# Kernel tuning notes

Measured on AMD Instinct MI355X. Metric: run time of the kernel, lower is better.

The kernel has to match this reference:

```python
import jax, jax.numpy as jnp
import numpy as np

N = 100000
NEG_SLOPE = 0.2
EPS = 1e-16


def gat_conv(x, edge_index, W, att_src, att_dst, bias, concat):
    # x: [N, Fin]; W: [Fin, H*C]; att_*: [H, C]; edge_index: [2, E] (with self loops)
    H, C = att_src.shape
    src, dst = edge_index[0], edge_index[1]
    h = (x @ W).reshape(-1, H, C)                       # [N, H, C]
    a_src = (h * att_src).sum(-1)                       # [N, H]
    a_dst = (h * att_dst).sum(-1)                       # [N, H]
    e = a_src[src] + a_dst[dst]                         # [E, H]
    e = jnp.where(e >= 0, e, NEG_SLOPE * e)             # LeakyReLU(0.2)
    # segment softmax over destination-node neighborhoods
    m = jax.ops.segment_max(e, dst, num_segments=N)     # [N, H]
    ex = jnp.exp(e - m[dst])
    denom = jax.ops.segment_sum(ex, dst, num_segments=N)
    alpha = ex / (denom[dst] + EPS)                     # [E, H]
    msg = h[src] * alpha[:, :, None]                    # [E, H, C]
    out = jax.ops.segment_sum(msg, dst, num_segments=N)  # [N, H, C]
    out = out.reshape(N, H * C) if concat else out.mean(axis=1)
    return out + bias


def setup_inputs() -> dict:
    key = jax.random.key(0)
    ks = jax.random.split(key, 10)
    Fin, Ch, Co, Hh = 256, 32, 64, 4
    E = 1600000
    x = jax.random.normal(ks[0], (N, Fin), dtype=jnp.float32)
    edge_index = jax.random.randint(ks[1], (2, E), 0, N, dtype=jnp.int64)
    s1 = 1.0 / np.sqrt(Fin)
    s2 = 1.0 / np.sqrt(Hh * Ch)
    W1 = jax.random.normal(ks[2], (Fin, Hh * Ch), dtype=jnp.float32) * s1
    att_src1 = jax.random.normal(ks[3], (Hh, Ch), dtype=jnp.float32) * (1.0 / np.sqrt(Ch))
    att_dst1 = jax.random.normal(ks[4], (Hh, Ch), dtype=jnp.float32) * (1.0 / np.sqrt(Ch))
    b1 = jnp.zeros((Hh * Ch,), dtype=jnp.float32)
    W2 = jax.random.normal(ks[5], (Hh * Ch, Co), dtype=jnp.float32) * s2
    att_src2 = jax.random.normal(ks[6], (1, Co), dtype=jnp.float32) * (1.0 / np.sqrt(Co))
    att_dst2 = jax.random.normal(ks[7], (1, Co), dtype=jnp.float32) * (1.0 / np.sqrt(Co))
    b2 = jnp.zeros((Co,), dtype=jnp.float32)
    return {"x": x, "edge_index": edge_index,
            "W1": W1, "att_src1": att_src1, "att_dst1": att_dst1, "b1": b1,
            "W2": W2, "att_src2": att_src2, "att_dst2": att_dst2, "b2": b2}


def reference(x, edge_index, W1, att_src1, att_dst1, b1, W2, att_src2, att_dst2, b2):
    # add self-loops (PyG GATConv default add_self_loops=True)
    loops = jnp.arange(N, dtype=edge_index.dtype)
    ei = jnp.concatenate([edge_index, jnp.stack([loops, loops])], axis=1)
    h = gat_conv(x, ei, W1, att_src1, att_dst1, b1, concat=True)
    h = jax.nn.elu(h)
    out = gat_conv(h, ei, W2, att_src2, att_dst2, b2, concat=False)
    return out
```

## Files before the change

kernel.cpp:

```cpp
#include <hip/hip_runtime.h>
#include <math.h>

typedef unsigned short ushort_t;
typedef unsigned int uint_t;
typedef __attribute__((ext_vector_type(8))) short short8;
typedef __attribute__((ext_vector_type(4))) float fx4;
typedef __attribute__((ext_vector_type(4))) uint_t uintx4;
typedef __attribute__((ext_vector_type(2))) uint_t uintx2;

__device__ __forceinline__ float bf16_to_f32(ushort_t u) {
    union { uint_t i; float f; } c;
    c.i = ((uint_t)u) << 16;
    return c.f;
}
__device__ __forceinline__ ushort_t f32_to_bf16(float f) {
    union { float f; uint_t i; } c;
    c.f = f;
    const uint_t x = c.i;
    return (ushort_t)((x + 0x7fffu + ((x >> 16) & 1u)) >> 16);
}
__device__ __forceinline__ void unpack_fma(uint_t w, float p, float& a0,
                                           float& a1) {
    union { uint_t i; float f; } lo, hi;
    lo.i = w << 16;
    hi.i = w & 0xffff0000u;
    a0 += p * lo.f;
    a1 += p * hi.f;
}

__global__ void convT_kernel(const float* __restrict__ W,
                             ushort_t* __restrict__ WT, int k, int m) {
    const int idx = blockIdx.x * 256 + threadIdx.x;
    if (idx >= k * m) return;
    const int mm = idx / k;
    const int kk = idx % k;
    WT[idx] = f32_to_bf16(W[(size_t)kk * m + mm]);
}

template <int TILES, bool A_F32, int K>
__global__ __launch_bounds__(256) void gemm_lds_kernel(
    const void* __restrict__ Avoid, const ushort_t* __restrict__ BT,
    ushort_t* __restrict__ C, int n) {
    constexpr int M = TILES * 16;
    constexpr int CH = K / 8;
    constexpr int NC = K / 32;
    __shared__ ushort_t lds[M * K];
    const int tid = threadIdx.x;

#pragma unroll
    for (int i = 0; i < (M * CH + 255) / 256; ++i) {
        const int idx = tid + i * 256;
        if (idx < M * CH) {
            const int row = idx / CH;
            const int c = idx - row * CH;
            *(short8*)&lds[(size_t)(row * CH + (c ^ (row & 7))) * 8] =
                *(const short8*)(BT + (size_t)row * K + c * 8);
        }
    }
    __syncthreads();

    const int wave = tid >> 6;
    const int lane = tid & 63;
    const int l15 = lane & 15;
    const int quad = lane >> 4;
    const int rowbase = blockIdx.x * 128 + wave * 32;
    const int r0 = min(rowbase + l15, n - 1);
    const int r1 = min(rowbase + 16 + l15, n - 1);
    const size_t off0 = (size_t)r0 * K + quad * 8;
    const size_t off1 = (size_t)r1 * K + quad * 8;

    fx4 acc[2][TILES];
#pragma unroll
    for (int rp = 0; rp < 2; ++rp)
#pragma unroll
        for (int t = 0; t < TILES; ++t) acc[rp][t] = (fx4){0.f, 0.f, 0.f, 0.f};

    fx4 c0a, c0b, c1a, c1b, n0a, n0b, n1a, n1b;
    short8 cb0, cb1, nb0, nb1;

    if constexpr (A_F32) {
        const float* A = (const float*)Avoid;
        c0a = *(const fx4*)(A + off0);
        c0b = *(const fx4*)(A + off0 + 4);
        c1a = *(const fx4*)(A + off1);
        c1b = *(const fx4*)(A + off1 + 4);
    } else {
        const ushort_t* A = (const ushort_t*)Avoid;
        cb0 = *(const short8*)(A + off0);
        cb1 = *(const short8*)(A + off1);
    }

#pragma unroll
    for (int kc = 0; kc < NC; ++kc) {
        if (kc + 1 < NC) {
            const int kd = (kc + 1) * 32;
            if constexpr (A_F32) {
                const float* A = (const float*)Avoid;
                n0a = *(const fx4*)(A + off0 + kd);
                n0b = *(const fx4*)(A + off0 + kd + 4);
                n1a = *(const fx4*)(A + off1 + kd);
                n1b = *(const fx4*)(A + off1 + kd + 4);
            } else {
                const ushort_t* A = (const ushort_t*)Avoid;
                nb0 = *(const short8*)(A + off0 + kd);
                nb1 = *(const short8*)(A + off1 + kd);
            }
        }
        short8 bf[TILES];
#pragma unroll
        for (int t = 0; t < TILES; ++t) {
            const int brow = t * 16 + l15;
            const int c = kc * 4 + quad;
            bf[t] = *(const short8*)&lds[(size_t)(brow * CH +
                                                  (c ^ (brow & 7))) * 8];
        }
        short8 af0, af1;
        if constexpr (A_F32) {
            union { short8 v; ushort_t u[8]; } u0, u1;
#pragma unroll
            for (int j = 0; j < 4; ++j) {
                u0.u[j] = f32_to_bf16(c0a[j]);
                u0.u[4 + j] = f32_to_bf16(c0b[j]);
                u1.u[j] = f32_to_bf16(c1a[j]);
                u1.u[4 + j] = f32_to_bf16(c1b[j]);
            }
            af0 = u0.v;
            af1 = u1.v;
        } else {
            af0 = cb0;
            af1 = cb1;
        }
#pragma unroll
        for (int t = 0; t < TILES; ++t) {
            acc[0][t] = __builtin_amdgcn_mfma_f32_16x16x32_bf16(af0, bf[t],
                                                                acc[0][t],
                                                                0, 0, 0);
            acc[1][t] = __builtin_amdgcn_mfma_f32_16x16x32_bf16(af1, bf[t],
                                                                acc[1][t],
                                                                0, 0, 0);
        }
        if (kc + 1 < NC) {
            if constexpr (A_F32) {
                c0a = n0a; c0b = n0b; c1a = n1a; c1b = n1b;
            } else {
                cb0 = nb0; cb1 = nb1;
            }
        }
    }

#pragma unroll
    for (int rp = 0; rp < 2; ++rp) {
        const int crow0 = rowbase + rp * 16 + quad * 4;
#pragma unroll
        for (int t = 0; t < TILES; ++t) {
#pragma unroll
            for (int r = 0; r < 4; ++r) {
                const int rr = crow0 + r;
                if (rr < n)
                    C[(size_t)rr * M + t * 16 + l15] =
                        f32_to_bf16(acc[rp][t][r]);
            }
        }
    }
}

template <int H, int C>
__global__ void att_kernel(const ushort_t* __restrict__ h,
                           const float* __restrict__ att_s,
                           const float* __restrict__ att_d,
                           float* __restrict__ as_, float* __restrict__ ad_,
                           int n) {
    const int idx = blockIdx.x * blockDim.x + threadIdx.x;
    if (idx >= n * H) return;
    const int node = idx / H;
    const int hh = idx % H;
    const ushort_t* hp = h + (size_t)node * H * C + hh * C;
    float s0 = 0.f, s1 = 0.f;
#pragma unroll
    for (int c = 0; c < C; ++c) {
        const float v = bf16_to_f32(hp[c]);
        s0 += v * att_s[hh * C + c];
        s1 += v * att_d[hh * C + c];
    }
    as_[idx] = s0;
    ad_[idx] = s1;
}

__global__ __launch_bounds__(1024) void hist_kernel(const int* __restrict__ dst,
                                                    int* __restrict__ histG,
                                                    int e, int chunk, int NB,
                                                    int G) {
    __shared__ int hl[512];
    for (int b = threadIdx.x; b < NB; b += 1024) hl[b] = 0;
    __syncthreads();
    const int g = blockIdx.x;
    const int lo = g * chunk;
    const int hi = min(lo + chunk, e);
    for (int i = lo + threadIdx.x; i < hi; i += 1024)
        atomicAdd(&hl[dst[i] >> 8], 1);
    __syncthreads();
    for (int b = threadIdx.x; b < NB; b += 1024) histG[b * G + g] = hl[b];
}

__global__ __launch_bounds__(1024) void scan1_kernel(const int* __restrict__ in,
                                                     int* __restrict__ out,
                                                     int* __restrict__ sums,
                                                     int n) {
    __shared__ int s[1024];
    const int t = threadIdx.x;
    const int i = blockIdx.x * 1024 + t;
    const int v = (i < n) ? in[i] : 0;
    s[t] = v;
    __syncthreads();
    for (int d = 1; d < 1024; d <<= 1) {
        const int x = (t >= d) ? s[t - d] : 0;
        __syncthreads();
        s[t] += x;
        __syncthreads();
    }
    if (i < n) out[i] = s[t] - v;
    if (t == 1023) sums[blockIdx.x] = s[1023];
}

__global__ __launch_bounds__(128) void scan2_kernel(int* sums, int nb) {
    __shared__ int s[128];
    const int t = threadIdx.x;
    const int v = (t < nb) ? sums[t] : 0;
    s[t] = v;
    __syncthreads();
    for (int d = 1; d < 128; d <<= 1) {
        const int x = (t >= d) ? s[t - d] : 0;
        __syncthreads();
        s[t] += x;
        __syncthreads();
    }
    if (t < nb) sums[t] = s[t] - v;
}

__global__ __launch_bounds__(1024) void scan3_kernel(int* __restrict__ out,
                                                     const int* __restrict__ sums,
                                                     int n) {
    const int i = blockIdx.x * 1024 + threadIdx.x;
    if (i < n) out[i] += sums[blockIdx.x];
}

__global__ __launch_bounds__(1024) void bin_kernel(const int* __restrict__ src,
                                                   const int* __restrict__ dst,
                                                   const int* __restrict__ base,
                                                   int2* __restrict__ binned,
                                                   int e, int chunk, int NB,
                                                   int G) {
    __shared__ int cur[512];
    const int g = blockIdx.x;
    for (int b = threadIdx.x; b < NB; b += 1024) cur[b] = base[b * G + g];
    __syncthreads();
    const int lo = g * chunk;
    const int hi = min(lo + chunk, e);
    for (int i = lo + threadIdx.x; i < hi; i += 1024) {
        const int d = dst[i];
        const int p = atomicAdd(&cur[d >> 8], 1);
        binned[p] = make_int2(src[i], d);
    }
}

#define BUILD_CAP 6144
__global__ __launch_bounds__(256) void build_kernel(
    const int2* __restrict__ binned, const int* __restrict__ base,
    int* __restrict__ csr, int* __restrict__ deg, int* __restrict__ offs,
    int e, int n, int NB, int G) {
    __shared__ int2 ep[BUILD_CAP];
    __shared__ int degL[256];
    __shared__ int offL[256];
    __shared__ int curL[256];
    const int b = blockIdx.x;
    const int tid = threadIdx.x;
    const int start = base[b * G];
    const int end = (b == NB - 1) ? e : base[(b + 1) * G];
    const int cnt = end - start;
    const bool stage = (cnt <= BUILD_CAP);
    degL[tid] = 0;
    if (stage)
        for (int i = tid; i < cnt; i += 256) ep[i] = binned[start + i];
    __syncthreads();
    if (stage) {
        for (int i = tid; i < cnt; i += 256) atomicAdd(&degL[ep[i].y & 255], 1);
    } else {
        for (int i = tid; i < cnt; i += 256)
            atomicAdd(&degL[binned[start + i].y & 255], 1);
    }
    __syncthreads();
    const int v = degL[tid];
    offL[tid] = v;
    __syncthreads();
    for (int d = 1; d < 256; d <<= 1) {
        const int x = (tid >= d) ? offL[tid - d] : 0;
        __syncthreads();
        offL[tid] += x;
        __syncthreads();
    }
    const int excl = offL[tid] - v;
    curL[tid] = excl;
    const int node = (b << 8) + tid;
    if (node < n) {
        deg[node] = v;
        offs[node] = start + excl;
    }
    __syncthreads();
    if (stage) {
        for (int i = tid; i < cnt; i += 256) {
            const int p = atomicAdd(&curL[ep[i].y & 255], 1);
            csr[start + p] = ep[i].x;
        }
    } else {
        for (int i = tid; i < cnt; i += 256) {
            const int2 pr = binned[start + i];
            const int p = atomicAdd(&curL[pr.y & 255], 1);
            csr[start + p] = pr.x;
        }
    }
}

template <int H, int C, bool DO_ELU, bool OUT_BF16>
__global__ __launch_bounds__(64) void agg_kernel(
    const ushort_t* __restrict__ h, const float* __restrict__ a_src,
    const float* __restrict__ a_dst, const int* __restrict__ csr,
    const int* __restrict__ offs, const int* __restrict__ deg,
    const float* __restrict__ bias, void* __restrict__ outv, int n) {
    constexpr int HC = H * C;
    constexpr int R = HC / 16;
    constexpr int RW = R / 2;
    constexpr int U = 4;
    const int lane = threadIdx.x;
    const int s = lane & 15;
    const int g = lane >> 4;
    const int dst = blockIdx.x * 4 + g;
    const int dstc = min(dst, n - 1);
    const int start = offs[dstc];
    const int dg = deg[dstc];
    const int ch0 = s * R;
    const int myh = (H > 1) ? (ch0 / C) : 0;
    const float advm = a_dst[dstc * H + myh];

    int dmax = dg;
    dmax = max(dmax, __shfl_xor(dmax, 16));
    dmax = max(dmax, __shfl_xor(dmax, 32));
    dmax = __builtin_amdgcn_readfirstlane(dmax);

    float acc[R];
#pragma unroll
    for (int r = 0; r < R; ++r) acc[r] = 0.f;
    float L = 0.f;

    {
        float e = a_src[dstc * H + myh] + advm;
        e = fmaxf(e, 0.2f * e);
        const float p = __expf(e);
        L += p;
        const ushort_t* hp = h + (size_t)((uint_t)dstc * HC) + ch0;
        if constexpr (RW == 4) {
            const uintx4 v = *(const uintx4*)hp;
#pragma unroll
            for (int w = 0; w < 4; ++w)
                unpack_fma(v[w], p, acc[2 * w], acc[2 * w + 1]);
        } else {
            const uintx2 v = *(const uintx2*)hp;
#pragma unroll
            for (int w = 0; w < 2; ++w)
                unpack_fma(v[w], p, acc[2 * w], acc[2 * w + 1]);
        }
    }

    const int dm1c = (dg > 0) ? dg - 1 : 0;

    for (int j0 = 0; j0 < dmax; j0 += U) {
        int sv[U];
#pragma unroll
        for (int u = 0; u < U; ++u)
            sv[u] = csr[start + min(j0 + u, dm1c)];
        float es[U];
#pragma unroll
        for (int u = 0; u < U; ++u) es[u] = a_src[sv[u] * H + myh];
        uint_t hv[U][RW];
#pragma unroll
        for (int u = 0; u < U; ++u) {
            const ushort_t* hp = h + (size_t)((uint_t)sv[u] * HC) + ch0;
            if constexpr (RW == 4) {
                const uintx4 v = *(const uintx4*)hp;
#pragma unroll
                for (int w = 0; w < 4; ++w) hv[u][w] = v[w];
            } else {
                const uintx2 v = *(const uintx2*)hp;
#pragma unroll
                for (int w = 0; w < 2; ++w) hv[u][w] = v[w];
            }
        }
        float p[U];
#pragma unroll
        for (int u = 0; u < U; ++u) {
            float e = es[u] + advm;
            e = fmaxf(e, 0.2f * e);
            const float pe = __expf(e);
            p[u] = (j0 + u < dg) ? pe : 0.f;
        }
#pragma unroll
        for (int u = 0; u < U; ++u) {
            L += p[u];
#pragma unroll
            for (int w = 0; w < RW; ++w)
                unpack_fma(hv[u][w], p[u], acc[2 * w], acc[2 * w + 1]);
        }
    }

    if (dst >= n) return;
    const float linv = 1.f / (L + 1e-16f);
    float r[R];
#pragma unroll
    for (int d = 0; d < R; ++d) {
        r[d] = acc[d] * linv + bias[ch0 + d];
        if (DO_ELU) r[d] = (r[d] > 0.f) ? r[d] : (__expf(r[d]) - 1.f);
    }
    if constexpr (OUT_BF16) {
        uintx4 o;
#pragma unroll
        for (int w = 0; w < 4; ++w)
            o[w] = (uint_t)f32_to_bf16(r[2 * w]) |
                   ((uint_t)f32_to_bf16(r[2 * w + 1]) << 16);
        *(uintx4*)((ushort_t*)outv + (size_t)dst * HC + ch0) = o;
    } else {
        fx4 o;
#pragma unroll
        for (int d = 0; d < 4; ++d) o[d] = r[d];
        *(fx4*)((float*)outv + (size_t)dst * HC + ch0) = o;
    }
}

extern "C" void kernel_launch(void* const* d_in, const int* in_sizes, int n_in,
                              void* d_out, int out_size, void* d_ws,
                              size_t ws_size, hipStream_t stream) {
    const float* x = (const float*)d_in[0];
    const int* ei = (const int*)d_in[1];
    const float* W1 = (const float*)d_in[2];
    const float* att_s1 = (const float*)d_in[3];
    const float* att_d1 = (const float*)d_in[4];
    const float* b1 = (const float*)d_in[5];
    const float* W2 = (const float*)d_in[6];
    const float* att_s2 = (const float*)d_in[7];
    const float* att_d2 = (const float*)d_in[8];
    const float* b2 = (const float*)d_in[9];

    const int N = in_sizes[0] / 256;
    const int E = in_sizes[1] / 2;
    const int* srcp = ei;
    const int* dstp = ei + E;

    const int NB = (N + 255) >> 8;
    const int G = 128;
    const int NBG = NB * G;
    const int chunk = (E + G - 1) / G;
    const int nbs = (NBG + 1023) / 1024;

    float* as1 = (float*)d_ws;
    float* ad1 = as1 + (size_t)N * 4;
    float* as2 = ad1 + (size_t)N * 4;
    float* ad2 = as2 + N;
    int* histG = (int*)(ad2 + N);
    int* base = histG + NBG;
    int* sums = base + NBG;
    int* deg = sums + 128;
    int* offs = deg + N;
    int* csr = offs + N;
    int2* binned = (int2*)(csr + E);
    ushort_t* h1 = (ushort_t*)binned;
    ushort_t* h2 = h1 + (size_t)N * 128;
    ushort_t* h1p = h2 + (size_t)N * 64;
    ushort_t* W1T = h1p + (size_t)N * 128;
    ushort_t* W2T = W1T + 128 * 256;

    convT_kernel<<<(256 * 128 + 255) / 256, 256, 0, stream>>>(W1, W1T, 256, 128);
    convT_kernel<<<(128 * 64 + 255) / 256, 256, 0, stream>>>(W2, W2T, 128, 64);

    hist_kernel<<<G, 1024, 0, stream>>>(dstp, histG, E, chunk, NB, G);
    scan1_kernel<<<nbs, 1024, 0, stream>>>(histG, base, sums, NBG);
    scan2_kernel<<<1, 128, 0, stream>>>(sums, nbs);
    scan3_kernel<<<nbs, 1024, 0, stream>>>(base, sums, NBG);
    bin_kernel<<<G, 1024, 0, stream>>>(srcp, dstp, base, binned, E, chunk, NB,
                                       G);
    build_kernel<<<NB, 256, 0, stream>>>(binned, base, csr, deg, offs, E, N,
                                         NB, G);

    const int gblk = (N + 127) / 128;
    const int ablk = (N + 3) / 4;

    gemm_lds_kernel<8, true, 256><<<gblk, 256, 0, stream>>>(x, W1T, h1, N);
    att_kernel<4, 32><<<(N * 4 + 255) / 256, 256, 0, stream>>>(h1, att_s1,
                                                               att_d1, as1,
                                                               ad1, N);
    agg_kernel<4, 32, true, true><<<ablk, 64, 0, stream>>>(h1, as1, ad1, csr,
                                                           offs, deg, b1, h1p,
                                                           N);

    gemm_lds_kernel<4, false, 128><<<gblk, 256, 0, stream>>>(h1p, W2T, h2, N);
    att_kernel<1, 64><<<(N + 255) / 256, 256, 0, stream>>>(h2, att_s2, att_d2,
                                                           as2, ad2, N);
    agg_kernel<1, 64, false, false><<<ablk, 64, 0, stream>>>(h2, as2, ad2,
                                                             csr, offs, deg,
                                                             b2, d_out, N);
}
```

Baseline: 394.3 us.

## Build CSR with global atomics and slice GEMM weight staging in LDS

Replaces the binned histogram/bin/build CSR construction with a simple degree count via global atomics, a scan over nodes, and an atomic-cursor scatter, removing the intermediate binned edge buffer and several kernels. The GEMM now loads the transposed weights into LDS in K-slices of 128, halving shared memory for the first layer and adding an occupancy hint. Global random atomics may contend more than LDS atomics, and neighbor order within a CSR row becomes nondeterministic.

```diff
diff --git a/kernel.cpp b/kernel.cpp
--- a/kernel.cpp
+++ b/kernel.cpp
@@ -37,28 +37,16 @@
     WT[idx] = f32_to_bf16(W[(size_t)kk * m + mm]);
 }
 
-template <int TILES, bool A_F32, int K>
-__global__ __launch_bounds__(256) void gemm_lds_kernel(
+template <int TILES, bool A_F32, int K, int KS>
+__global__ __launch_bounds__(256, 4) void gemm_lds_kernel(
     const void* __restrict__ Avoid, const ushort_t* __restrict__ BT,
     ushort_t* __restrict__ C, int n) {
     constexpr int M = TILES * 16;
-    constexpr int CH = K / 8;
+    constexpr int CHS = KS / 8;
+    constexpr int NCS = KS / 32;
     constexpr int NC = K / 32;
-    __shared__ ushort_t lds[M * K];
+    __shared__ ushort_t lds[M * KS];
     const int tid = threadIdx.x;
-
-#pragma unroll
-    for (int i = 0; i < (M * CH + 255) / 256; ++i) {
-        const int idx = tid + i * 256;
-        if (idx < M * CH) {
-            const int row = idx / CH;
-            const int c = idx - row * CH;
-            *(short8*)&lds[(size_t)(row * CH + (c ^ (row & 7))) * 8] =
-                *(const short8*)(BT + (size_t)row * K + c * 8);
-        }
-    }
-    __syncthreads();
-
     const int wave = tid >> 6;
     const int lane = tid & 63;
     const int l15 = lane & 15;
@@ -91,59 +79,74 @@
     }
 
 #pragma unroll
-    for (int kc = 0; kc < NC; ++kc) {
-        if (kc + 1 < NC) {
-            const int kd = (kc + 1) * 32;
+    for (int ks = 0; ks < K; ks += KS) {
+        if (ks) __syncthreads();
+#pragma unroll
+        for (int i = 0; i < (M * CHS + 255) / 256; ++i) {
+            const int idx = tid + i * 256;
+            if (idx < M * CHS) {
+                const int row = idx / CHS;
+                const int c = idx - row * CHS;
+                *(short8*)&lds[(size_t)(row * CHS + (c ^ (row & 7))) * 8] =
+                    *(const short8*)(BT + (size_t)row * K + ks + c * 8);
+            }
+        }
+        __syncthreads();
+
+#pragma unroll
+        for (int kc = 0; kc < NCS; ++kc) {
+            const int kg = ks / 32 + kc;
+            if (kg + 1 < NC) {
+                const int kd = (kg + 1) * 32;
+                if constexpr (A_F32) {
+                    const float* A = (const float*)Avoid;
+                    n0a = *(const fx4*)(A + off0 + kd);
+                    n0b = *(const fx4*)(A + off0 + kd + 4);
+                    n1a = *(const fx4*)(A + off1 + kd);
+                    n1b = *(const fx4*)(A + off1 + kd + 4);
+                } else {
+                    const ushort_t* A = (const ushort_t*)Avoid;
+                    nb0 = *(const short8*)(A + off0 + kd);
+                    nb1 = *(const short8*)(A + off1 + kd);
+                }
+            }
+            short8 bf[TILES];
+#pragma unroll
+            for (int t = 0; t < TILES; ++t) {
+                const int brow = t * 16 + l15;
+                const int c = kc * 4 + quad;
+                bf[t] = *(const short8*)&lds[(size_t)(brow * CHS +
+                                                      (c ^ (brow & 7))) * 8];
+            }
+            short8 af0, af1;
             if constexpr (A_F32) {
-                const float* A = (const float*)Avoid;
-                n0a = *(const fx4*)(A + off0 + kd);
-                n0b = *(const fx4*)(A + off0 + kd + 4);
-                n1a = *(const fx4*)(A + off1 + kd);
-                n1b = *(const fx4*)(A + off1 + kd + 4);
+                union { short8 v; ushort_t u[8]; } u0, u1;
+#pragma unroll
+                for (int j = 0; j < 4; ++j) {
+                    u0.u[j] = f32_to_bf16(c0a[j]);
+                    u0.u[4 + j] = f32_to_bf16(c0b[j]);
+                    u1.u[j] = f32_to_bf16(c1a[j]);
+                    u1.u[4 + j] = f32_to_bf16(c1b[j]);
+                }
+                af0 = u0.v;
+                af1 = u1.v;
             } else {
-                const ushort_t* A = (const ushort_t*)Avoid;
-                nb0 = *(const short8*)(A + off0 + kd);
-                nb1 = *(const short8*)(A + off1 + kd);
-            }
-        }
-        short8 bf[TILES];
-#pragma unroll
-        for (int t = 0; t < TILES; ++t) {
-            const int brow = t * 16 + l15;
-            const int c = kc * 4 + quad;
-            bf[t] = *(const short8*)&lds[(size_t)(brow * CH +
-                                                  (c ^ (brow & 7))) * 8];
-        }
-        short8 af0, af1;
-        if constexpr (A_F32) {
-            union { short8 v; ushort_t u[8]; } u0, u1;
-#pragma unroll
-            for (int j = 0; j < 4; ++j) {
-                u0.u[j] = f32_to_bf16(c0a[j]);
-                u0.u[4 + j] = f32_to_bf16(c0b[j]);
-                u1.u[j] = f32_to_bf16(c1a[j]);
-                u1.u[4 + j] = f32_to_bf16(c1b[j]);
-            }
-            af0 = u0.v;
-            af1 = u1.v;
-        } else {
-            af0 = cb0;
-            af1 = cb1;
-        }
-#pragma unroll
-        for (int t = 0; t < TILES; ++t) {
-            acc[0][t] = __builtin_amdgcn_mfma_f32_16x16x32_bf16(af0, bf[t],
-                                                                acc[0][t],
-                                                                0, 0, 0);
-            acc[1][t] = __builtin_amdgcn_mfma_f32_16x16x32_bf16(af1, bf[t],
-                                                                acc[1][t],
-                                                                0, 0, 0);
-        }
-        if (kc + 1 < NC) {
-            if constexpr (A_F32) {
-                c0a = n0a; c0b = n0b; c1a = n1a; c1b = n1b;
-            } else {
-                cb0 = nb0; cb1 = nb1;
+                af0 = cb0;
+                af1 = cb1;
+            }
+#pragma unroll
+            for (int t = 0; t < TILES; ++t) {
+                acc[0][t] = __builtin_amdgcn_mfma_f32_16x16x32_bf16(
+                    af0, bf[t], acc[0][t], 0, 0, 0);
+                acc[1][t] = __builtin_amdgcn_mfma_f32_16x16x32_bf16(
+                    af1, bf[t], acc[1][t], 0, 0, 0);
+            }
+            if (kg + 1 < NC) {
+                if constexpr (A_F32) {
+                    c0a = n0a; c0b = n0b; c1a = n1a; c1b = n1b;
+                } else {
+                    cb0 = nb0; cb1 = nb1;
+                }
             }
         }
     }
@@ -186,20 +189,17 @@
     ad_[idx] = s1;
 }
 
-__global__ __launch_bounds__(1024) void hist_kernel(const int* __restrict__ dst,
-                                                    int* __restrict__ histG,
-                                                    int e, int chunk, int NB,
-                                                    int G) {
-    __shared__ int hl[512];
-    for (int b = threadIdx.x; b < NB; b += 1024) hl[b] = 0;
-    __syncthreads();
-    const int g = blockIdx.x;
-    const int lo = g * chunk;
-    const int hi = min(lo + chunk, e);
-    for (int i = lo + threadIdx.x; i < hi; i += 1024)
-        atomicAdd(&hl[dst[i] >> 8], 1);
-    __syncthreads();
-    for (int b = threadIdx.x; b < NB; b += 1024) histG[b * G + g] = hl[b];
+__global__ __launch_bounds__(256) void zero_kernel(int* __restrict__ p,
+                                                   int n) {
+    const int i = blockIdx.x * 256 + threadIdx.x;
+    if (i < n) p[i] = 0;
+}
+
+__global__ __launch_bounds__(256) void deg_kernel(const int* __restrict__ dst,
+                                                  int* __restrict__ deg,
+                                                  int e) {
+    for (int i = blockIdx.x * 256 + threadIdx.x; i < e; i += gridDim.x * 256)
+        atomicAdd(&deg[dst[i]], 1);
 }
 
 __global__ __launch_bounds__(1024) void scan1_kernel(const int* __restrict__ in,
@@ -237,86 +237,24 @@
     if (t < nb) sums[t] = s[t] - v;
 }
 
-__global__ __launch_bounds__(1024) void scan3_kernel(int* __restrict__ out,
-                                                     const int* __restrict__ sums,
-                                                     int n) {
+__global__ __launch_bounds__(1024) void scan3w_kernel(
+    int* __restrict__ out, int* __restrict__ cur,
+    const int* __restrict__ sums, int n) {
     const int i = blockIdx.x * 1024 + threadIdx.x;
-    if (i < n) out[i] += sums[blockIdx.x];
-}
-
-__global__ __launch_bounds__(1024) void bin_kernel(const int* __restrict__ src,
-                                                   const int* __restrict__ dst,
-                                                   const int* __restrict__ base,
-                                                   int2* __restrict__ binned,
-                                                   int e, int chunk, int NB,
-                                                   int G) {
-    __shared__ int cur[512];
-    const int g = blockIdx.x;
-    for (int b = threadIdx.x; b < NB; b += 1024) cur[b] = base[b * G + g];
-    __syncthreads();
-    const int lo = g * chunk;
-    const int hi = min(lo + chunk, e);
-    for (int i = lo + threadIdx.x; i < hi; i += 1024) {
+    if (i < n) {
+        const int v = out[i] + sums[blockIdx.x];
+        out[i] = v;
+        cur[i] = v;
+    }
+}
+
+__global__ __launch_bounds__(256) void scatter_kernel(
+    const int* __restrict__ src, const int* __restrict__ dst,
+    int* __restrict__ cur, int* __restrict__ csr, int e) {
+    for (int i = blockIdx.x * 256 + threadIdx.x; i < e; i += gridDim.x * 256) {
         const int d = dst[i];
-        const int p = atomicAdd(&cur[d >> 8], 1);
-        binned[p] = make_int2(src[i], d);
-    }
-}
-
-#define BUILD_CAP 6144
-__global__ __launch_bounds__(256) void build_kernel(
-    const int2* __restrict__ binned, const int* __restrict__ base,
-    int* __restrict__ csr, int* __restrict__ deg, int* __restrict__ offs,
-    int e, int n, int NB, int G) {
-    __shared__ int2 ep[BUILD_CAP];
-    __shared__ int degL[256];
-    __shared__ int offL[256];
-    __shared__ int curL[256];
-    const int b = blockIdx.x;
-    const int tid = threadIdx.x;
-    const int start = base[b * G];
-    const int end = (b == NB - 1) ? e : base[(b + 1) * G];
-    const int cnt = end - start;
-    const bool stage = (cnt <= BUILD_CAP);
-    degL[tid] = 0;
-    if (stage)
-        for (int i = tid; i < cnt; i += 256) ep[i] = binned[start + i];
-    __syncthreads();
-    if (stage) {
-        for (int i = tid; i < cnt; i += 256) atomicAdd(&degL[ep[i].y & 255], 1);
-    } else {
-        for (int i = tid; i < cnt; i += 256)
-            atomicAdd(&degL[binned[start + i].y & 255], 1);
-    }
-    __syncthreads();
-    const int v = degL[tid];
-    offL[tid] = v;
-    __syncthreads();
-    for (int d = 1; d < 256; d <<= 1) {
-        const int x = (tid >= d) ? offL[tid - d] : 0;
-        __syncthreads();
-        offL[tid] += x;
-        __syncthreads();
-    }
-    const int excl = offL[tid] - v;
-    curL[tid] = excl;
-    const int node = (b << 8) + tid;
-    if (node < n) {
-        deg[node] = v;
-        offs[node] = start + excl;
-    }
-    __syncthreads();
-    if (stage) {
-        for (int i = tid; i < cnt; i += 256) {
-            const int p = atomicAdd(&curL[ep[i].y & 255], 1);
-            csr[start + p] = ep[i].x;
-        }
-    } else {
-        for (int i = tid; i < cnt; i += 256) {
-            const int2 pr = binned[start + i];
-            const int p = atomicAdd(&curL[pr.y & 255], 1);
-            csr[start + p] = pr.x;
-        }
+        const int p = atomicAdd(&cur[d], 1);
+        csr[p] = src[i];
     }
 }
 
@@ -453,24 +391,18 @@
     const int* srcp = ei;
     const int* dstp = ei + E;
 
-    const int NB = (N + 255) >> 8;
-    const int G = 128;
-    const int NBG = NB * G;
-    const int chunk = (E + G - 1) / G;
-    const int nbs = (NBG + 1023) / 1024;
+    const int nbs = (N + 1023) / 1024;
 
     float* as1 = (float*)d_ws;
     float* ad1 = as1 + (size_t)N * 4;
     float* as2 = ad1 + (size_t)N * 4;
     float* ad2 = as2 + N;
-    int* histG = (int*)(ad2 + N);
-    int* base = histG + NBG;
-    int* sums = base + NBG;
-    int* deg = sums + 128;
+    int* deg = (int*)(ad2 + N);
     int* offs = deg + N;
-    int* csr = offs + N;
-    int2* binned = (int2*)(csr + E);
-    ushort_t* h1 = (ushort_t*)binned;
+    int* cur = offs + N;
+    int* sums = cur + N;
+    int* csr = sums + 128;
+    ushort_t* h1 = (ushort_t*)(csr + E);
     ushort_t* h2 = h1 + (size_t)N * 128;
     ushort_t* h1p = h2 + (size_t)N * 64;
     ushort_t* W1T = h1p + (size_t)N * 128;
@@ -479,19 +411,18 @@
     convT_kernel<<<(256 * 128 + 255) / 256, 256, 0, stream>>>(W1, W1T, 256, 128);
     convT_kernel<<<(128 * 64 + 255) / 256, 256, 0, stream>>>(W2, W2T, 128, 64);
 
-    hist_kernel<<<G, 1024, 0, stream>>>(dstp, histG, E, chunk, NB, G);
-    scan1_kernel<<<nbs, 1024, 0, stream>>>(histG, base, sums, NBG);
+    zero_kernel<<<(N + 255) / 256, 256, 0, stream>>>(deg, N);
+    deg_kernel<<<2048, 256, 0, stream>>>(dstp, deg, E);
+    scan1_kernel<<<nbs, 1024, 0, stream>>>(deg, offs, sums, N);
     scan2_kernel<<<1, 128, 0, stream>>>(sums, nbs);
-    scan3_kernel<<<nbs, 1024, 0, stream>>>(base, sums, NBG);
-    bin_kernel<<<G, 1024, 0, stream>>>(srcp, dstp, base, binned, E, chunk, NB,
-                                       G);
-    build_kernel<<<NB, 256, 0, stream>>>(binned, base, csr, deg, offs, E, N,
-                                         NB, G);
+    scan3w_kernel<<<nbs, 1024, 0, stream>>>(offs, cur, sums, N);
+    scatter_kernel<<<2048, 256, 0, stream>>>(srcp, dstp, cur, csr, E);
 
     const int gblk = (N + 127) / 128;
     const int ablk = (N + 3) / 4;
 
-    gemm_lds_kernel<8, true, 256><<<gblk, 256, 0, stream>>>(x, W1T, h1, N);
+    gemm_lds_kernel<8, true, 256, 128><<<gblk, 256, 0, stream>>>(x, W1T, h1,
+                                                                 N);
     att_kernel<4, 32><<<(N * 4 + 255) / 256, 256, 0, stream>>>(h1, att_s1,
                                                                att_d1, as1,
                                                                ad1, N);
@@ -499,7 +430,8 @@
                                                            offs, deg, b1, h1p,
                                                            N);
 
-    gemm_lds_kernel<4, false, 128><<<gblk, 256, 0, stream>>>(h1p, W2T, h2, N);
+    gemm_lds_kernel<4, false, 128, 128><<<gblk, 256, 0, stream>>>(h1p, W2T,
+                                                                  h2, N);
     att_kernel<1, 64><<<(N + 255) / 256, 256, 0, stream>>>(h2, att_s2, att_d2,
                                                            as2, ad2, N);
     agg_kernel<1, 64, false, false><<<ablk, 64, 0, stream>>>(h2, as2, ad2,
```

New measurement: 532.7 us. +35.1%, slower.
